# Performance work log

Hardware: AMD Instinct MI355X
Metric: run time of the kernel (lower is better)

Reference implementation:

```python
import jax, jax.numpy as jnp
import numpy as np

EMBED_DIMS = 256
NUM_GROUPS = 8
NUM_LEVELS = 4
NUM_CAMS = 6
NUM_LEARNABLE_PTS = 6
FIX_SCALE = np.array([[0,0,0],[0.45,0,0],[-0.45,0,0],[0,0.45,0],[0,-0.45,0],[0,0,0.45],[0,0,-0.45]], dtype=np.float32)
NUM_PTS = len(FIX_SCALE) + NUM_LEARNABLE_PTS  # 13
GROUP_DIMS = EMBED_DIMS // NUM_GROUPS


def safe_sigmoid(x):
    return jax.nn.sigmoid(jnp.clip(x, -9.21, 9.21))


def get_rotation_matrix(q):
    # q: [..., 4] quaternion (w, x, y, z), normalized first (GaussianFormer convention)
    q = q / jnp.linalg.norm(q, axis=-1, keepdims=True)
    w, x, y, z = q[..., 0], q[..., 1], q[..., 2], q[..., 3]
    R = jnp.stack([
        jnp.stack([1 - 2 * (y * y + z * z), 2 * (x * y - w * z), 2 * (x * z + w * y)], axis=-1),
        jnp.stack([2 * (x * y + w * z), 1 - 2 * (x * x + z * z), 2 * (y * z - w * x)], axis=-1),
        jnp.stack([2 * (x * z - w * y), 2 * (y * z + w * x), 1 - 2 * (x * x + y * y)], axis=-1),
    ], axis=-2)
    return R  # [..., 3, 3]


def key_points_generator(anchor, instance_feature, W_learn, b_learn):
    bs, num_anchor = anchor.shape[:2]
    fix_scale = jnp.asarray(FIX_SCALE, anchor.dtype)  # [7, 3]
    scale = jnp.broadcast_to(fix_scale[None, None], (bs, num_anchor, fix_scale.shape[0], 3))
    learnable = safe_sigmoid((instance_feature @ W_learn + b_learn)
                             .reshape(bs, num_anchor, NUM_LEARNABLE_PTS, 3)) - 0.5
    scale = jnp.concatenate([scale, learnable], axis=-2)         # [bs, na, P, 3]
    gs_scales = anchor[..., None, 3:6]                           # [bs, na, 1, 3]
    key_points = scale * gs_scales                               # [bs, na, P, 3]
    rot_T = jnp.swapaxes(get_rotation_matrix(anchor[..., 6:10]), -1, -2)  # [bs, na, 3, 3]
    key_points = jnp.einsum('bnij,bnpj->bnpi', rot_T, key_points)
    return key_points + anchor[..., None, :3]                    # [bs, na, P, 3]


def project_points(key_points, projection_mat, image_wh):
    # key_points [bs, na, P, 3], projection_mat [bs, cams, 4, 4]
    ones = jnp.ones_like(key_points[..., :1])
    pts4 = jnp.concatenate([key_points, ones], axis=-1)          # [bs, na, P, 4]
    p2d = jnp.einsum('bcij,bnpj->bcnpi', projection_mat, pts4)   # [bs, cams, na, P, 4]
    p2d = p2d[..., :2] / jnp.maximum(p2d[..., 2:3], 1e-5)
    p2d = p2d / image_wh[:, :, None, None]
    return jnp.clip(p2d, 0.0, 0.9999)                            # [bs, cams, na, P, 2]


def bilinear_sample(feat, pts):
    # feat [bs, cams, C, H, W], pts [bs, P, cams, 2] normalized to [0,1]
    bs, cams, C, H, W = feat.shape
    x = pts[..., 0] * W - 0.5
    y = pts[..., 1] * H - 0.5
    x0 = jnp.floor(x); y0 = jnp.floor(y)
    wx = x - x0; wy = y - y0
    x0i = x0.astype(jnp.int32); y0i = y0.astype(jnp.int32)
    feat_f = jnp.transpose(feat, (0, 1, 3, 4, 2)).reshape(bs, cams, H * W, C)
    b_idx = jnp.arange(bs)[:, None, None]
    c_idx = jnp.arange(cams)[None, None, :]

    def gather(yy, xx):
        valid = (yy >= 0) & (yy < H) & (xx >= 0) & (xx < W)
        yc = jnp.clip(yy, 0, H - 1)
        xc = jnp.clip(xx, 0, W - 1)
        v = feat_f[b_idx, c_idx, yc * W + xc]                    # [bs, P, cams, C]
        return v * valid[..., None].astype(v.dtype)

    v00 = gather(y0i, x0i)
    v01 = gather(y0i, x0i + 1)
    v10 = gather(y0i + 1, x0i)
    v11 = gather(y0i + 1, x0i + 1)
    wx = wx[..., None]; wy = wy[..., None]
    return (v00 * (1 - wx) * (1 - wy) + v01 * wx * (1 - wy)
            + v10 * (1 - wx) * wy + v11 * wx * wy)               # [bs, P, cams, C]


def deformable_aggregate(feature_maps, points_2d, weights):
    # points_2d [bs, P, cams, 2]; weights [bs, P, cams, levels, groups]
    bs, P = points_2d.shape[:2]
    out = jnp.zeros((bs, P, NUM_GROUPS, GROUP_DIMS), points_2d.dtype)
    for l, feat in enumerate(feature_maps):
        samp = bilinear_sample(feat, points_2d)                  # [bs, P, cams, C]
        samp = samp.reshape(bs, P, feat.shape[1], NUM_GROUPS, GROUP_DIMS)
        out = out + jnp.einsum('bpcgd,bpcg->bpgd', samp, weights[:, :, :, l, :])
    return out.reshape(bs, P, EMBED_DIMS)


def _forward(pts3d, instance_feature, anchor, feat0, feat1, feat2, feat3,
             projection_mat, image_wh, W_learn, b_learn, W_wts, b_wts, W_out, b_out):
    bs, num_anchor = instance_feature.shape[:2]
    key_points = key_points_generator(anchor, instance_feature, W_learn, b_learn)
    # softmax weights over cams*levels*pts jointly, per group
    w = (instance_feature @ W_wts + b_wts).reshape(bs, num_anchor, -1, NUM_GROUPS)
    w = jax.nn.softmax(w, axis=-2)
    w = w.reshape(bs, num_anchor, NUM_CAMS, NUM_LEVELS, NUM_PTS, NUM_GROUPS)
    w = jnp.transpose(w, (0, 1, 4, 2, 3, 5)).reshape(bs, num_anchor * NUM_PTS, NUM_CAMS, NUM_LEVELS, NUM_GROUPS)
    p2d = project_points(key_points, projection_mat, image_wh)   # [bs, cams, na, P, 2]
    p2d = jnp.transpose(p2d, (0, 2, 3, 1, 4)).reshape(bs, num_anchor * NUM_PTS, NUM_CAMS, 2)
    feats = deformable_aggregate([feat0, feat1, feat2, feat3], p2d, w)
    feats = feats.reshape(bs, num_anchor, NUM_PTS, EMBED_DIMS).sum(axis=2)
    output = feats @ W_out + b_out
    return output + instance_feature


def setup_inputs() -> dict:
    key = jax.random.key(0)
    ks = jax.random.split(key, 16)
    bs, na = 1, 4096
    shapes = [(bs, 6, 256, 64, 176), (bs, 6, 256, 32, 88), (bs, 6, 256, 16, 44), (bs, 6, 256, 8, 22)]
    inp = {
        'pts3d': jax.random.normal(ks[0], (100000, 3), jnp.float32),
        'instance_feature': jax.random.normal(ks[1], (bs, na, EMBED_DIMS), jnp.float32),
        'anchor': jax.random.normal(ks[2], (bs, na, 11), jnp.float32),
        'feat0': jax.random.normal(ks[3], shapes[0], jnp.float32),
        'feat1': jax.random.normal(ks[4], shapes[1], jnp.float32),
        'feat2': jax.random.normal(ks[5], shapes[2], jnp.float32),
        'feat3': jax.random.normal(ks[6], shapes[3], jnp.float32),
        'projection_mat': jax.random.normal(ks[7], (bs, NUM_CAMS, 4, 4), jnp.float32),
        'image_wh': jnp.broadcast_to(jnp.array([704.0, 256.0], jnp.float32), (bs, NUM_CAMS, 2)),
        'W_learn': jax.random.normal(ks[8], (EMBED_DIMS, NUM_LEARNABLE_PTS * 3), jnp.float32) * 0.02,
        'b_learn': jnp.zeros((NUM_LEARNABLE_PTS * 3,), jnp.float32),
        'W_wts': jax.random.normal(ks[9], (EMBED_DIMS, NUM_GROUPS * NUM_CAMS * NUM_LEVELS * NUM_PTS), jnp.float32) * 0.02,
        'b_wts': jnp.zeros((NUM_GROUPS * NUM_CAMS * NUM_LEVELS * NUM_PTS,), jnp.float32),
        'W_out': jax.random.normal(ks[10], (EMBED_DIMS, EMBED_DIMS), jnp.float32) * 0.02,
        'b_out': jnp.zeros((EMBED_DIMS,), jnp.float32),
    }
    return inp


def reference(pts3d, instance_feature, anchor, feat0, feat1, feat2, feat3,
              projection_mat, image_wh, W_learn, b_learn, W_wts, b_wts, W_out, b_out):
    return _forward(pts3d, instance_feature, anchor, feat0, feat1, feat2, feat3,
                    projection_mat, image_wh, W_learn, b_learn, W_wts, b_wts, W_out, b_out)
```

## Files before the change

kernel.cpp:

```cpp
#include <hip/hip_runtime.h>
#include <math.h>


#define FT_L0 0
#define FT_L1 17301504
#define FT_L2 21626880
#define FT_L3 22708224
#define WS_LOGB 5744640
#define WS_FEATB 10856448
#define WS_LEARN 11380736
#define WS_AB 11454464
#define WS_BB 11978752
#define WS_WOB 12306432

typedef float v2f __attribute__((ext_vector_type(2)));
typedef __attribute__((ext_vector_type(8))) short bf16x8;
typedef __attribute__((ext_vector_type(4))) float f32x4;

__device__ const float FIXS[7][3] = {
    {0.f, 0.f, 0.f},  {0.45f, 0.f, 0.f}, {-0.45f, 0.f, 0.f}, {0.f, 0.45f, 0.f},
    {0.f, -0.45f, 0.f}, {0.f, 0.f, 0.45f}, {0.f, 0.f, -0.45f}};

__device__ __forceinline__ unsigned int f2bf(float f) {
  unsigned int u = __float_as_uint(f);
  u += 0x7fffu + ((u >> 16) & 1u);
  return u >> 16;
}
__device__ __forceinline__ float bf2f(unsigned short u) {
  return __uint_as_float(((unsigned int)u) << 16);
}

__global__ __launch_bounds__(256) void k_transpose_all(
    const float* __restrict__ f0, const float* __restrict__ f1,
    const float* __restrict__ f2, const float* __restrict__ f3,
    unsigned char* __restrict__ featF) {
  const int bx = blockIdx.x;
  const float* src;
  unsigned char* dst;
  int H, W, xt;
  if (bx < 6)       { src = f0; dst = featF + FT_L0; H = 64; W = 176; xt = bx * 32; }
  else if (bx < 9)  { src = f1; dst = featF + FT_L1; H = 32; W = 88;  xt = (bx - 6) * 32; }
  else if (bx < 11) { src = f2; dst = featF + FT_L2; H = 16; W = 44;  xt = (bx - 9) * 32; }
  else              { src = f3; dst = featF + FT_L3; H = 8;  W = 22;  xt = 0; }
  const int y = blockIdx.y;
  if (y >= H) return;
  __shared__ float tile[32][33];
  const int tid = threadIdx.x;
  const int i = tid & 31;
  const int j = tid >> 5;
  const int c = blockIdx.z >> 3;
  const int cht = (blockIdx.z & 7) * 32;
#pragma unroll
  for (int jj = j; jj < 32; jj += 8) {
    int x = xt + i;
    float v = 0.f;
    if (x < W) v = src[((c * 256 + cht + jj) * H + y) * W + x];
    tile[jj][i] = v;
  }
  __syncthreads();
  const int q = tid & 7;
  const int xw = tid >> 3;
  const int x = xt + xw;
  if (x < W) {
    const float v0 = tile[q * 4 + 0][xw];
    const float v1 = tile[q * 4 + 1][xw];
    const float v2 = tile[q * 4 + 2][xw];
    const float v3 = tile[q * 4 + 3][xw];
    int pk = __builtin_amdgcn_cvt_pk_fp8_f32(v0, v1, 0, false);
    pk = __builtin_amdgcn_cvt_pk_fp8_f32(v2, v3, pk, true);
    *(unsigned int*)(dst + (((c * H + y) * W + x) * 256) + cht + q * 4) =
        (unsigned int)pk;
  }
}

__global__ __launch_bounds__(256) void k_prep_pack(
    const float* __restrict__ iw, const float* __restrict__ Ww,
    const float* __restrict__ Wl, const float* __restrict__ Wo,
    unsigned short* __restrict__ Ab, unsigned short* __restrict__ Bb,
    unsigned short* __restrict__ Wob) {
  __shared__ unsigned short tile[32][33];
  const int tid = threadIdx.x;
  const int bx = blockIdx.x;
  if (bx < 1024) {
    const int i = bx * 256 + tid;
    const float4 v = ((const float4*)iw)[i];
    uint2 o;
    o.x = f2bf(v.x) | (f2bf(v.y) << 16);
    o.y = f2bf(v.z) | (f2bf(v.w) << 16);
    ((uint2*)Ab)[i] = o;
    return;
  }
  const int i = tid & 31;
  const int r = tid >> 5;
  if (bx < 1664) {
    const int idx = bx - 1024;
    const int j0 = (idx % 80) * 32;
    const int k0 = (idx / 80) * 32;
#pragma unroll
    for (int rr = r; rr < 32; rr += 8) {
      const int k = k0 + rr, j = j0 + i;
      float v = 0.f;
      if (j < 2496) v = Ww[k * 2496 + j];
      else if (j < 2514) v = Wl[k * 18 + (j - 2496)];
      tile[rr][i] = (unsigned short)f2bf(v);
    }
    __syncthreads();
#pragma unroll
    for (int rr = r; rr < 32; rr += 8)
      Bb[(j0 + rr) * 256 + k0 + i] = tile[i][rr];
  } else {
    const int idx = bx - 1664;
    const int j0 = (idx & 7) * 32;
    const int k0 = (idx >> 3) * 32;
#pragma unroll
    for (int rr = r; rr < 32; rr += 8)
      tile[rr][i] = (unsigned short)f2bf(Wo[(k0 + rr) * 256 + j0 + i]);
    __syncthreads();
#pragma unroll
    for (int rr = r; rr < 32; rr += 8)
      Wob[(j0 + rr) * 256 + k0 + i] = tile[i][rr];
  }
}

__global__ __launch_bounds__(256) void k_wts_mfma(
    const unsigned short* __restrict__ Ab, const unsigned short* __restrict__ Bb,
    const float* __restrict__ b_wts, const float* __restrict__ b_learn,
    unsigned short* __restrict__ logitsB, float* __restrict__ learn) {
  const int tid = threadIdx.x;
  const int w = tid >> 6, lane = tid & 63;
  const int ml = lane & 15, q = lane >> 4;
  const int n0 = blockIdx.x * 64;
  const int m0 = blockIdx.y * 64;
  f32x4 acc[4] = {{0.f, 0.f, 0.f, 0.f}, {0.f, 0.f, 0.f, 0.f},
                  {0.f, 0.f, 0.f, 0.f}, {0.f, 0.f, 0.f, 0.f}};
  const unsigned short* Ap = Ab + (m0 + w * 16 + ml) * 256 + q * 8;
  const unsigned short* Bp = Bb + (n0 + ml) * 256 + q * 8;
#pragma unroll
  for (int kk = 0; kk < 8; ++kk) {
    const bf16x8 a = *(const bf16x8*)(Ap + kk * 32);
#pragma unroll
    for (int nt = 0; nt < 4; ++nt) {
      const bf16x8 b = *(const bf16x8*)(Bp + nt * 16 * 256 + kk * 32);
      acc[nt] = __builtin_amdgcn_mfma_f32_16x16x32_bf16(a, b, acc[nt], 0, 0, 0);
    }
  }
  const int rowb = m0 + w * 16 + q * 4;
#pragma unroll
  for (int nt = 0; nt < 4; ++nt) {
    const int col = n0 + nt * 16 + ml;
    if (col < 2496) {
      const float b = b_wts[col];
#pragma unroll
      for (int r = 0; r < 4; ++r)
        logitsB[(rowb + r) * 2496 + col] = (unsigned short)f2bf(acc[nt][r] + b);
    } else if (col < 2514) {
      const float b = b_learn[col - 2496];
#pragma unroll
      for (int r = 0; r < 4; ++r) {
        float v = fminf(fmaxf(acc[nt][r] + b, -9.21f), 9.21f);
        learn[(rowb + r) * 18 + (col - 2496)] = 1.f / (1.f + expf(-v)) - 0.5f;
      }
    }
  }
}

__device__ __forceinline__ void fma16(const uint4 u, const float s, v2f* acc) {
  const v2f w = {s, s};
  v2f t;
  t = __builtin_amdgcn_cvt_pk_f32_fp8((int)u.x, false);
  asm("v_pk_fma_f32 %0, %1, %2, %0" : "+v"(acc[0]) : "v"(t), "v"(w));
  t = __builtin_amdgcn_cvt_pk_f32_fp8((int)u.x, true);
  asm("v_pk_fma_f32 %0, %1, %2, %0" : "+v"(acc[1]) : "v"(t), "v"(w));
  t = __builtin_amdgcn_cvt_pk_f32_fp8((int)u.y, false);
  asm("v_pk_fma_f32 %0, %1, %2, %0" : "+v"(acc[2]) : "v"(t), "v"(w));
  t = __builtin_amdgcn_cvt_pk_f32_fp8((int)u.y, true);
  asm("v_pk_fma_f32 %0, %1, %2, %0" : "+v"(acc[3]) : "v"(t), "v"(w));
  t = __builtin_amdgcn_cvt_pk_f32_fp8((int)u.z, false);
  asm("v_pk_fma_f32 %0, %1, %2, %0" : "+v"(acc[4]) : "v"(t), "v"(w));
  t = __builtin_amdgcn_cvt_pk_f32_fp8((int)u.z, true);
  asm("v_pk_fma_f32 %0, %1, %2, %0" : "+v"(acc[5]) : "v"(t), "v"(w));
  t = __builtin_amdgcn_cvt_pk_f32_fp8((int)u.w, false);
  asm("v_pk_fma_f32 %0, %1, %2, %0" : "+v"(acc[6]) : "v"(t), "v"(w));
  t = __builtin_amdgcn_cvt_pk_f32_fp8((int)u.w, true);
  asm("v_pk_fma_f32 %0, %1, %2, %0" : "+v"(acc[7]) : "v"(t), "v"(w));
}

__global__ __launch_bounds__(256, 8) void k_sample(
    const float* __restrict__ anchor, const unsigned short* __restrict__ logitsB,
    const float* __restrict__ learn_g, const unsigned char* __restrict__ featF,
    const float* __restrict__ proj, const float* __restrict__ wh,
    unsigned short* __restrict__ featsB) {
  const int n = blockIdx.x;
  const int tid = threadIdx.x;
  const int lane = tid & 63;
  const int wave = tid >> 6;
  __shared__ unsigned short s_w[8 * 328];
  __shared__ float s_p2d[78][2];
  __shared__ float s_learn[18];
  __shared__ union SmpLds {
    struct { int4 off[320]; float4 wt[320]; } tab;
    float red[4][256];
  } u;

  for (int i = tid; i < 2496; i += 256) {
    const int s = i >> 3, g = i & 7;
    const int c = s / 52;
    const int r = s - c * 52;
    const int l = r / 13;
    const int p = r - l * 13;
    s_w[g * 328 + (p * 6 + c) * 4 + l] = logitsB[n * 2496 + i];
  }
  if (tid < 64) s_w[(tid >> 3) * 328 + 312 + (tid & 7)] = 0;
  if (tid < 18) s_learn[tid] = learn_g[n * 18 + tid];
  __syncthreads();

#pragma unroll
  for (int gg = 0; gg < 2; ++gg) {
    unsigned short* row = &s_w[(wave * 2 + gg) * 328];
    float l[5];
    float mx = -1e30f;
#pragma unroll
    for (int i = 0; i < 5; ++i) {
      const int s = lane + i * 64;
      l[i] = (s < 312) ? bf2f(row[s]) : -1e30f;
      mx = fmaxf(mx, l[i]);
    }
    for (int off = 32; off; off >>= 1) mx = fmaxf(mx, __shfl_xor(mx, off));
    float sum = 0.f;
#pragma unroll
    for (int i = 0; i < 5; ++i) {
      l[i] = __expf(l[i] - mx);
      sum += l[i];
    }
    for (int off = 32; off; off >>= 1) sum += __shfl_xor(sum, off);
    const float inv = 1.f / sum;
#pragma unroll
    for (int i = 0; i < 5; ++i) {
      const int s = lane + i * 64;
      if (s < 312) row[s] = (unsigned short)f2bf(l[i] * inv);
    }
  }

  if (tid < 78) {
    const int p = tid / 6, c = tid % 6;
    const float* an = anchor + n * 11;
    float qw = an[6], qx = an[7], qy = an[8], qz = an[9];
    const float qinv = 1.f / sqrtf(qw * qw + qx * qx + qy * qy + qz * qz);
    qw *= qinv; qx *= qinv; qy *= qinv; qz *= qinv;
    const float R00 = 1.f - 2.f * (qy * qy + qz * qz), R01 = 2.f * (qx * qy - qw * qz), R02 = 2.f * (qx * qz + qw * qy);
    const float R10 = 2.f * (qx * qy + qw * qz), R11 = 1.f - 2.f * (qx * qx + qz * qz), R12 = 2.f * (qy * qz - qw * qx);
    const float R20 = 2.f * (qx * qz - qw * qy), R21 = 2.f * (qy * qz + qw * qx), R22 = 1.f - 2.f * (qx * qx + qy * qy);
    float s0, s1, s2;
    if (p < 7) {
      s0 = FIXS[p][0]; s1 = FIXS[p][1]; s2 = FIXS[p][2];
    } else {
      const int b = (p - 7) * 3;
      s0 = s_learn[b]; s1 = s_learn[b + 1]; s2 = s_learn[b + 2];
    }
    const float vx = s0 * an[3], vy = s1 * an[4], vz = s2 * an[5];
    const float kx = R00 * vx + R10 * vy + R20 * vz + an[0];
    const float ky = R01 * vx + R11 * vy + R21 * vz + an[1];
    const float kz = R02 * vx + R12 * vy + R22 * vz + an[2];
    const float* P = proj + c * 16;
    const float h0 = P[0] * kx + P[1] * ky + P[2] * kz + P[3];
    const float h1 = P[4] * kx + P[5] * ky + P[6] * kz + P[7];
    const float h2 = P[8] * kx + P[9] * ky + P[10] * kz + P[11];
    const float zz = fmaxf(h2, 1e-5f);
    float px = h0 / zz / wh[c * 2 + 0];
    float py = h1 / zz / wh[c * 2 + 1];
    px = fminf(fmaxf(px, 0.f), 0.9999f);
    py = fminf(fmaxf(py, 0.f), 0.9999f);
    s_p2d[tid][0] = px;
    s_p2d[tid][1] = py;
  }
  __syncthreads();

  {
    constexpr int LBB[4] = {FT_L0, FT_L1, FT_L2, FT_L3};
    constexpr int CSB[4] = {2883584, 720896, 180224, 45056};
    for (int t = tid; t < 320; t += 256) {
      const int pc = t >> 2, l = t & 3;
      if (pc >= 78) {
        u.tab.off[t] = make_int4(0, 0, 0, 0);
        u.tab.wt[t] = make_float4(0.f, 0.f, 0.f, 0.f);
        continue;
      }
      const int c = pc % 6;
      const int H = 64 >> l, W = 176 >> l;
      const float fx = s_p2d[pc][0] * (float)W - 0.5f;
      const float fy = s_p2d[pc][1] * (float)H - 0.5f;
      const float x0f = floorf(fx), y0f = floorf(fy);
      const float wx = fx - x0f, wy = fy - y0f;
      const int x0 = (int)x0f, y0 = (int)y0f;
      const float mx0 = (x0 >= 0) ? 1.f : 0.f;
      const float mx1 = (x0 + 1 < W) ? 1.f : 0.f;
      const float my0 = (y0 >= 0) ? 1.f : 0.f;
      const float my1 = (y0 + 1 < H) ? 1.f : 0.f;
      const int cx0 = max(x0, 0), cx1 = min(x0 + 1, W - 1);
      const int cy0 = max(y0, 0), cy1 = min(y0 + 1, H - 1);
      const int base = LBB[l] + c * CSB[l];
      int4 o;
      o.x = base + (cy0 * W + cx0) * 256;
      o.y = base + (cy0 * W + cx1) * 256;
      o.z = base + (cy1 * W + cx0) * 256;
      o.w = base + (cy1 * W + cx1) * 256;
      u.tab.off[t] = o;
      float4 w4;
      w4.x = (1.f - wx) * (1.f - wy) * mx0 * my0;
      w4.y = wx * (1.f - wy) * mx1 * my0;
      w4.z = (1.f - wx) * wy * mx0 * my1;
      w4.w = wx * wy * mx1 * my1;
      u.tab.wt[t] = w4;
    }
  }
  __syncthreads();

  const int q = lane >> 4;
  const int ql = lane & 15;
  const int chb = ql * 16;
  const int g = ql >> 1;
  v2f acc[8];
#pragma unroll
  for (int k = 0; k < 8; ++k) acc[k] = (v2f){0.f, 0.f};
  const unsigned char* fb = featF;
  const unsigned short* wrow = &s_w[g * 328];
  const int pcb = wave * 4 + q;
#pragma unroll
  for (int it = 0; it < 5; ++it) {
    const int pc = pcb + it * 16;
    const int t0 = pc * 4;
    const uint2 wq = *(const uint2*)&wrow[t0];
    float wgl[4];
    wgl[0] = __uint_as_float(wq.x << 16);
    wgl[1] = __uint_as_float(wq.x & 0xffff0000u);
    wgl[2] = __uint_as_float(wq.y << 16);
    wgl[3] = __uint_as_float(wq.y & 0xffff0000u);
#pragma unroll
    for (int l4 = 0; l4 < 4; ++l4) {
      const int t = t0 + l4;
      const int4 o = u.tab.off[t];
      const float4 bw = u.tab.wt[t];
      const float wg = wgl[l4];
      const uint4 u0 = *(const uint4*)(fb + (o.x + chb));
      const uint4 u1 = *(const uint4*)(fb + (o.y + chb));
      const uint4 u2 = *(const uint4*)(fb + (o.z + chb));
      const uint4 u3 = *(const uint4*)(fb + (o.w + chb));
      fma16(u0, bw.x * wg, acc);
      fma16(u1, bw.y * wg, acc);
      fma16(u2, bw.z * wg, acc);
      fma16(u3, bw.w * wg, acc);
    }
  }
#pragma unroll
  for (int k = 0; k < 8; ++k) {
    v2f b;
    b.x = __shfl_xor(acc[k].x, 16);
    b.y = __shfl_xor(acc[k].y, 16);
    acc[k] += b;
    b.x = __shfl_xor(acc[k].x, 32);
    b.y = __shfl_xor(acc[k].y, 32);
    acc[k] += b;
  }
  __syncthreads();
  if (lane < 16) {
    float* dst = &u.red[wave][ql * 16];
    *(float4*)(dst + 0)  = make_float4(acc[0].x, acc[0].y, acc[1].x, acc[1].y);
    *(float4*)(dst + 4)  = make_float4(acc[2].x, acc[2].y, acc[3].x, acc[3].y);
    *(float4*)(dst + 8)  = make_float4(acc[4].x, acc[4].y, acc[5].x, acc[5].y);
    *(float4*)(dst + 12) = make_float4(acc[6].x, acc[6].y, acc[7].x, acc[7].y);
  }
  __syncthreads();
  {
    const float sum = u.red[0][tid] + u.red[1][tid] + u.red[2][tid] + u.red[3][tid];
    featsB[n * 256 + tid] = (unsigned short)f2bf(sum);
  }
}

__global__ __launch_bounds__(256) void k_out_mfma(
    const unsigned short* __restrict__ Ab, const unsigned short* __restrict__ Bb,
    const float* __restrict__ bias, const float* __restrict__ resid,
    float* __restrict__ out) {
  const int tid = threadIdx.x;
  const int w = tid >> 6, lane = tid & 63;
  const int ml = lane & 15, q = lane >> 4;
  const int n0 = blockIdx.x * 64;
  const int m0 = blockIdx.y * 64;
  f32x4 acc[4] = {{0.f, 0.f, 0.f, 0.f}, {0.f, 0.f, 0.f, 0.f},
                  {0.f, 0.f, 0.f, 0.f}, {0.f, 0.f, 0.f, 0.f}};
  const unsigned short* Ap = Ab + (m0 + w * 16 + ml) * 256 + q * 8;
  const unsigned short* Bp = Bb + (n0 + ml) * 256 + q * 8;
#pragma unroll
  for (int kk = 0; kk < 8; ++kk) {
    const bf16x8 a = *(const bf16x8*)(Ap + kk * 32);
#pragma unroll
    for (int nt = 0; nt < 4; ++nt) {
      const bf16x8 b = *(const bf16x8*)(Bp + nt * 16 * 256 + kk * 32);
      acc[nt] = __builtin_amdgcn_mfma_f32_16x16x32_bf16(a, b, acc[nt], 0, 0, 0);
    }
  }
  const int rowb = m0 + w * 16 + q * 4;
#pragma unroll
  for (int nt = 0; nt < 4; ++nt) {
    const int col = n0 + nt * 16 + ml;
    const float b = bias[col];
#pragma unroll
    for (int r = 0; r < 4; ++r) {
      const int row = rowb + r;
      out[row * 256 + col] = acc[nt][r] + b + resid[row * 256 + col];
    }
  }
}

extern "C" void kernel_launch(void* const* d_in, const int* in_sizes, int n_in,
                              void* d_out, int out_size, void* d_ws, size_t ws_size,
                              hipStream_t stream) {
  (void)in_sizes; (void)n_in; (void)out_size; (void)ws_size;
  const float* iw      = (const float*)d_in[1];
  const float* anchor  = (const float*)d_in[2];
  const float* f0      = (const float*)d_in[3];
  const float* f1      = (const float*)d_in[4];
  const float* f2      = (const float*)d_in[5];
  const float* f3      = (const float*)d_in[6];
  const float* proj    = (const float*)d_in[7];
  const float* wh      = (const float*)d_in[8];
  const float* W_learn = (const float*)d_in[9];
  const float* b_learn = (const float*)d_in[10];
  const float* W_wts   = (const float*)d_in[11];
  const float* b_wts   = (const float*)d_in[12];
  const float* W_out   = (const float*)d_in[13];
  const float* b_out   = (const float*)d_in[14];
  float* out = (float*)d_out;
  float* ws = (float*)d_ws;
  unsigned char*  featF   = (unsigned char*)ws;
  unsigned short* logitsB = (unsigned short*)(ws + WS_LOGB);
  unsigned short* featsB  = (unsigned short*)(ws + WS_FEATB);
  float*          learn   = ws + WS_LEARN;
  unsigned short* Ab      = (unsigned short*)(ws + WS_AB);
  unsigned short* Bb      = (unsigned short*)(ws + WS_BB);
  unsigned short* Wob     = (unsigned short*)(ws + WS_WOB);

  k_transpose_all<<<dim3(12, 64, 48), 256, 0, stream>>>(f0, f1, f2, f3, featF);
  k_prep_pack<<<1728, 256, 0, stream>>>(iw, W_wts, W_learn, W_out, Ab, Bb, Wob);
  k_wts_mfma<<<dim3(40, 64), 256, 0, stream>>>(Ab, Bb, b_wts, b_learn, logitsB, learn);
  k_sample<<<4096, 256, 0, stream>>>(anchor, logitsB, learn, featF, proj, wh, featsB);
  k_out_mfma<<<dim3(4, 64), 256, 0, stream>>>(featsB, Wob, b_out, iw, out);
}
```

Measured before the change: 305.4 us.

## Pre-swizzle bf16 GEMM operands into MFMA fragment order and drop inline-asm FMA

The prep kernel now writes the activation and weight bf16 matrices in a tiled layout that matches the 16x16x32 MFMA lane fragment order. Each lane in the GEMM can then load its fragment from contiguous memory (lane*8) instead of strided row reads, which coalesces the loads. Separately, the fp8 accumulate helper swaps hand-written v_pk_fma_f32 inline asm for plain vector multiply-add, so the compiler can schedule it. That relies on the compiler still emitting packed FMA and may cost rounding parity if it emits a separate multiply and add.

```diff
diff --git a/kernel.cpp b/kernel.cpp
--- a/kernel.cpp
+++ b/kernel.cpp
@@ -87,7 +87,12 @@
     uint2 o;
     o.x = f2bf(v.x) | (f2bf(v.y) << 16);
     o.y = f2bf(v.z) | (f2bf(v.w) << 16);
-    ((uint2*)Ab)[i] = o;
+    const int mtile = i >> 10;
+    const int ml = (i >> 6) & 15;
+    const int kk = (i & 63) >> 3;
+    const int q = (i >> 1) & 3;
+    const int j = (i & 1) * 4;
+    *(uint2*)&Ab[mtile * 4096 + kk * 512 + q * 128 + ml * 8 + j] = o;
     return;
   }
   const int i = tid & 31;
@@ -98,16 +103,25 @@
     const int k0 = (idx / 80) * 32;
 #pragma unroll
     for (int rr = r; rr < 32; rr += 8) {
-      const int k = k0 + rr, j = j0 + i;
+      const int k = k0 + rr, jc = j0 + i;
       float v = 0.f;
-      if (j < 2496) v = Ww[k * 2496 + j];
-      else if (j < 2514) v = Wl[k * 18 + (j - 2496)];
+      if (jc < 2496) v = Ww[k * 2496 + jc];
+      else if (jc < 2514) v = Wl[k * 18 + (jc - 2496)];
       tile[rr][i] = (unsigned short)f2bf(v);
     }
     __syncthreads();
-#pragma unroll
-    for (int rr = r; rr < 32; rr += 8)
-      Bb[(j0 + rr) * 256 + k0 + i] = tile[i][rr];
+    const int jn = tid >> 3;
+    const int kq = tid & 7;
+    const int ncol = j0 + jn;
+    const int k = k0 + kq * 4;
+    const int ntile = ncol >> 4, mln = ncol & 15;
+    const int kkn = k >> 5, qn = (k >> 3) & 3, jj = k & 7;
+    unsigned int h0 = (unsigned int)tile[kq * 4 + 0][jn] |
+                      ((unsigned int)tile[kq * 4 + 1][jn] << 16);
+    unsigned int h1 = (unsigned int)tile[kq * 4 + 2][jn] |
+                      ((unsigned int)tile[kq * 4 + 3][jn] << 16);
+    *(uint2*)&Bb[ntile * 4096 + kkn * 512 + qn * 128 + mln * 8 + jj] =
+        make_uint2(h0, h1);
   } else {
     const int idx = bx - 1664;
     const int j0 = (idx & 7) * 32;
@@ -133,14 +147,14 @@
   const int m0 = blockIdx.y * 64;
   f32x4 acc[4] = {{0.f, 0.f, 0.f, 0.f}, {0.f, 0.f, 0.f, 0.f},
                   {0.f, 0.f, 0.f, 0.f}, {0.f, 0.f, 0.f, 0.f}};
-  const unsigned short* Ap = Ab + (m0 + w * 16 + ml) * 256 + q * 8;
-  const unsigned short* Bp = Bb + (n0 + ml) * 256 + q * 8;
+  const unsigned short* Ap = Ab + (blockIdx.y * 4 + w) * 4096 + lane * 8;
+  const unsigned short* Bp = Bb + blockIdx.x * 4 * 4096 + lane * 8;
 #pragma unroll
   for (int kk = 0; kk < 8; ++kk) {
-    const bf16x8 a = *(const bf16x8*)(Ap + kk * 32);
+    const bf16x8 a = *(const bf16x8*)(Ap + kk * 512);
 #pragma unroll
     for (int nt = 0; nt < 4; ++nt) {
-      const bf16x8 b = *(const bf16x8*)(Bp + nt * 16 * 256 + kk * 32);
+      const bf16x8 b = *(const bf16x8*)(Bp + nt * 4096 + kk * 512);
       acc[nt] = __builtin_amdgcn_mfma_f32_16x16x32_bf16(a, b, acc[nt], 0, 0, 0);
     }
   }
@@ -166,23 +180,14 @@
 
 __device__ __forceinline__ void fma16(const uint4 u, const float s, v2f* acc) {
   const v2f w = {s, s};
-  v2f t;
-  t = __builtin_amdgcn_cvt_pk_f32_fp8((int)u.x, false);
-  asm("v_pk_fma_f32 %0, %1, %2, %0" : "+v"(acc[0]) : "v"(t), "v"(w));
-  t = __builtin_amdgcn_cvt_pk_f32_fp8((int)u.x, true);
-  asm("v_pk_fma_f32 %0, %1, %2, %0" : "+v"(acc[1]) : "v"(t), "v"(w));
-  t = __builtin_amdgcn_cvt_pk_f32_fp8((int)u.y, false);
-  asm("v_pk_fma_f32 %0, %1, %2, %0" : "+v"(acc[2]) : "v"(t), "v"(w));
-  t = __builtin_amdgcn_cvt_pk_f32_fp8((int)u.y, true);
-  asm("v_pk_fma_f32 %0, %1, %2, %0" : "+v"(acc[3]) : "v"(t), "v"(w));
-  t = __builtin_amdgcn_cvt_pk_f32_fp8((int)u.z, false);
-  asm("v_pk_fma_f32 %0, %1, %2, %0" : "+v"(acc[4]) : "v"(t), "v"(w));
-  t = __builtin_amdgcn_cvt_pk_f32_fp8((int)u.z, true);
-  asm("v_pk_fma_f32 %0, %1, %2, %0" : "+v"(acc[5]) : "v"(t), "v"(w));
-  t = __builtin_amdgcn_cvt_pk_f32_fp8((int)u.w, false);
-  asm("v_pk_fma_f32 %0, %1, %2, %0" : "+v"(acc[6]) : "v"(t), "v"(w));
-  t = __builtin_amdgcn_cvt_pk_f32_fp8((int)u.w, true);
-  asm("v_pk_fma_f32 %0, %1, %2, %0" : "+v"(acc[7]) : "v"(t), "v"(w));
+  acc[0] += __builtin_amdgcn_cvt_pk_f32_fp8((int)u.x, false) * w;
+  acc[1] += __builtin_amdgcn_cvt_pk_f32_fp8((int)u.x, true) * w;
+  acc[2] += __builtin_amdgcn_cvt_pk_f32_fp8((int)u.y, false) * w;
+  acc[3] += __builtin_amdgcn_cvt_pk_f32_fp8((int)u.y, true) * w;
+  acc[4] += __builtin_amdgcn_cvt_pk_f32_fp8((int)u.z, false) * w;
+  acc[5] += __builtin_amdgcn_cvt_pk_f32_fp8((int)u.z, true) * w;
+  acc[6] += __builtin_amdgcn_cvt_pk_f32_fp8((int)u.w, false) * w;
+  acc[7] += __builtin_amdgcn_cvt_pk_f32_fp8((int)u.w, true) * w;
 }
 
 __global__ __launch_bounds__(256, 8) void k_sample(
```

Result: faster. 272.0 us (-10.9%).
